# Performance work log

Hardware: AMD Instinct MI355X
Metric: run time of the kernel (lower is better)

Reference implementation:

```python
import jax, jax.numpy as jnp
import numpy as np

B, IN, H0, H1, OUT = 4096, 1024, 4096, 4096, 1024
QMAX = 127.0


def setup_inputs() -> dict:
    key = jax.random.key(0)
    k0, k1, k2, k3 = jax.random.split(key, 4)
    x = jax.random.normal(k0, (B, IN), dtype=jnp.float32)
    # Linear weights hold already-quantized integer values (module casts .int())
    W0 = jax.random.randint(k1, (H0, IN + 1), -127, 128).astype(jnp.int32)
    W1 = jax.random.randint(k2, (H1, H0 + 1), -127, 128).astype(jnp.int32)
    W2 = jax.random.randint(k3, (OUT, H1 + 1), -127, 128).astype(jnp.int32)
    return {
        "x": x,
        "a_in0": jnp.float32(4.0), "a_w0": jnp.float32(0.05),
        "a_in2": jnp.float32(50.0), "a_w2": jnp.float32(0.05),
        "a_in4": jnp.float32(50.0), "a_w4": jnp.float32(0.05),
        "W0": W0, "W1": W1, "W2": W2,
    }


def _quant(x, amax):
    # clamp(round(x * 127/amax), -127, 127) -> int32
    return jnp.clip(jnp.round(x * (QMAX / amax)), -QMAX, QMAX).astype(jnp.int32)


def _qlinear(x, W, a_in, a_w):
    q = _quant(x, a_in)                                   # [B, K] int32
    ones = jnp.ones((q.shape[0], 1), dtype=jnp.int32)     # folded bias column
    q = jnp.concatenate([q, ones], axis=1)                # [B, K+1]
    acc = q @ W.T                                         # int32 GEMM [B, N]
    return acc.astype(jnp.float32) * (a_w * a_in / (QMAX * QMAX))


def reference(x, a_in0, a_w0, a_in2, a_w2, a_in4, a_w4, W0, W1, W2):
    x = x.reshape(x.shape[0], -1)
    x = _qlinear(x, W0, a_in0, a_w0)
    x = jax.nn.relu(x)
    x = _qlinear(x, W1, a_in2, a_w2)
    x = jax.nn.relu(x)
    x = _qlinear(x, W2, a_in4, a_w4)
    return x
```

## Files before the change

kernel.cpp:

```cpp
#include <hip/hip_runtime.h>

#define QMAX 127.0f

typedef int v4i __attribute__((ext_vector_type(4)));

__device__ __forceinline__ void gload_lds16(const void* g, void* l) {
  __builtin_amdgcn_global_load_lds(
      (const __attribute__((address_space(1))) void*)g,
      (__attribute__((address_space(3))) void*)l, 16, 0, 0);
}

__global__ void quant_x_kernel(const float* __restrict__ x,
                               signed char* __restrict__ q,
                               const float* __restrict__ pAin, int n4) {
  int t = blockIdx.x * blockDim.x + threadIdx.x;
  if (t >= n4) return;
  float s = QMAX / pAin[0];
  float4 v = reinterpret_cast<const float4*>(x)[t];
  int q0 = (int)fminf(fmaxf(rintf(v.x * s), -QMAX), QMAX);
  int q1 = (int)fminf(fmaxf(rintf(v.y * s), -QMAX), QMAX);
  int q2 = (int)fminf(fmaxf(rintf(v.z * s), -QMAX), QMAX);
  int q3 = (int)fminf(fmaxf(rintf(v.w * s), -QMAX), QMAX);
  unsigned packed = (unsigned)(q0 & 0xff) | ((unsigned)(q1 & 0xff) << 8) |
                    ((unsigned)(q2 & 0xff) << 16) | ((unsigned)(q3 & 0xff) << 24);
  reinterpret_cast<unsigned*>(q)[t] = packed;
}

__global__ void pack_w_kernel(const int* __restrict__ W,
                              signed char* __restrict__ W8,
                              int* __restrict__ bias,
                              unsigned total, int kshift) {
  unsigned t = blockIdx.x * blockDim.x + threadIdx.x;
  if (t >= total) return;
  unsigned row = t >> kshift;
  unsigned j = t & ((1u << kshift) - 1u);
  unsigned K = 4u << kshift;
  size_t srcBase = (size_t)row * (size_t)(K + 1) + (size_t)j * 4;
  int b0 = W[srcBase + 0], b1 = W[srcBase + 1], b2 = W[srcBase + 2], b3 = W[srcBase + 3];
  unsigned packed = (unsigned)(b0 & 0xff) | ((unsigned)(b1 & 0xff) << 8) |
                    ((unsigned)(b2 & 0xff) << 16) | ((unsigned)(b3 & 0xff) << 24);
  reinterpret_cast<unsigned*>(W8)[t] = packed;
  if (j == 0) bias[row] = W[(size_t)row * (K + 1) + K];
}


#define FENCE() asm volatile("" ::: "memory")
#define BARRIER()                      \
  do {                                 \
    FENCE();                           \
    __builtin_amdgcn_s_barrier();      \
    FENCE();                           \
  } while (0)
#define LGK0() asm volatile("s_waitcnt lgkmcnt(0)" ::: "memory")
#define VMC6() asm volatile("s_waitcnt vmcnt(6)" ::: "memory")
#define VMC0() asm volatile("s_waitcnt vmcnt(0)" ::: "memory")

#define STAGE_A(bf, h, t)                                                     \
  do {                                                                        \
    const signed char* _g = gA + (size_t)((h) * 128) * K + (size_t)(t) * 128; \
    signed char* _l = ldsA + (bf) * 32768 + (h) * 16384 + ldsThr;             \
    gload_lds16(_g, _l);                                                      \
    gload_lds16(_g + (size_t)8 * K, _l + 1024);                               \
  } while (0)

#define STAGE_B(bf, h, t)                                                     \
  do {                                                                        \
    const signed char* _g = gB + (size_t)((h) * 128) * K + (size_t)(t) * 128; \
    signed char* _l = ldsB + (bf) * 32768 + (h) * 16384 + ldsThr;             \
    gload_lds16(_g, _l);                                                      \
    gload_lds16(_g + (size_t)8 * K, _l + 1024);                               \
  } while (0)

#define LDA(bf, qm)                                                           \
  do {                                                                        \
    _Pragma("unroll") for (int m = 0; m < 4; ++m) {                           \
      int row = wm * 128 + (qm) * 64 + m * 16 + l15;                          \
      _Pragma("unroll") for (int kk = 0; kk < 2; ++kk) {                      \
        int off = (kk * 64 + hi * 16) ^ ((row & 7) << 4);                     \
        aR[m][kk] = *(const v4i*)(ldsA + (bf) * 32768 + row * 128 + off);     \
      }                                                                       \
    }                                                                         \
  } while (0)

#define LDB(bf)                                                               \
  do {                                                                        \
    _Pragma("unroll") for (int n = 0; n < 4; ++n) {                           \
      int row = wn * 64 + n * 16 + l15;                                       \
      _Pragma("unroll") for (int kk = 0; kk < 2; ++kk) {                      \
        int off = (kk * 64 + hi * 16) ^ ((row & 7) << 4);                     \
        bR[n][kk] = *(const v4i*)(ldsB + (bf) * 32768 + row * 128 + off);     \
      }                                                                       \
    }                                                                         \
  } while (0)

#define MFMAQ(qm, qn)                                                         \
  do {                                                                        \
    __builtin_amdgcn_s_setprio(1);                                            \
    _Pragma("unroll") for (int m = 0; m < 4; ++m)                             \
    _Pragma("unroll") for (int n = 0; n < 2; ++n)                             \
    _Pragma("unroll") for (int kk = 0; kk < 2; ++kk)                          \
      acc[(qm) * 4 + m][(qn) * 2 + n] = __builtin_amdgcn_mfma_i32_16x16x64_i8(\
          aR[m][kk], bR[(qn) * 2 + n][kk], acc[(qm) * 4 + m][(qn) * 2 + n],   \
          0, 0, 0);                                                           \
    __builtin_amdgcn_s_setprio(0);                                            \
  } while (0)

__global__ __launch_bounds__(512, 2)
void qgemm256_kernel(const signed char* __restrict__ A,
                     const signed char* __restrict__ Bw,
                     const int* __restrict__ bias,
                     signed char* __restrict__ O,
                     int N, int K, int nbn,
                     const float* __restrict__ pAin,
                     const float* __restrict__ pAw,
                     const float* __restrict__ pAnext) {
  extern __shared__ signed char lds[];
  signed char* ldsA = lds;
  signed char* ldsB = lds + 65536;

  const int nwg = gridDim.x, bid = blockIdx.x, per = nwg >> 3;
  const int swz = (bid & 7) * per + (bid >> 3);
  const int brow = swz / nbn, bcol = swz - brow * nbn;
  const int browBase = brow << 8, bcolBase = bcol << 8;

  const int tid = threadIdx.x;
  const int lane = tid & 63, l15 = lane & 15, hi = lane >> 4;
  const int wid = tid >> 6, wm = wid >> 2, wn = wid & 3;

  const int rloc = (wid << 4) + (lane >> 3);
  const int csrc = (lane & 7) ^ ((lane >> 3) & 7);
  const signed char* gA = A + (size_t)(browBase + rloc) * K + csrc * 16;
  const signed char* gB = Bw + (size_t)(bcolBase + rloc) * K + csrc * 16;
  const int ldsThr = (wid << 11) + lane * 16;

  v4i acc[8][4] = {};
  v4i aR[4][2], bR[4][2];

  const int nk = K >> 7, niter = nk >> 1, nkm = nk - 1;

  STAGE_B(0, 0, 0); STAGE_B(0, 1, 0); STAGE_A(0, 0, 0); STAGE_A(0, 1, 0);
  STAGE_B(1, 0, 1); STAGE_B(1, 1, 1); STAGE_A(1, 0, 1);
  VMC6();
  BARRIER();

#pragma unroll 1
  for (int i = 0; i < niter; ++i) {
    const int t1 = 2 * i + 1;
    const int tE = (2 * i + 2) & nkm;
    const int tO = (2 * i + 3) & nkm;
    LDA(0, 0); LDB(0);
    STAGE_A(1, 1, t1);
    BARRIER(); LGK0();
    MFMAQ(0, 0);
    BARRIER();
    STAGE_B(0, 0, tE);
    BARRIER();
    MFMAQ(0, 1);
    BARRIER();
    LDA(0, 1);
    STAGE_B(0, 1, tE);
    BARRIER(); LGK0();
    MFMAQ(1, 0);
    BARRIER();
    STAGE_A(0, 0, tE);
    VMC6();
    BARRIER();
    MFMAQ(1, 1);
    BARRIER();
    LDA(1, 0); LDB(1);
    STAGE_A(0, 1, tE);
    BARRIER(); LGK0();
    MFMAQ(0, 0);
    BARRIER();
    STAGE_B(1, 0, tO);
    BARRIER();
    MFMAQ(0, 1);
    BARRIER();
    LDA(1, 1);
    STAGE_B(1, 1, tO);
    BARRIER(); LGK0();
    MFMAQ(1, 0);
    BARRIER();
    STAGE_A(1, 0, tO);
    VMC6();
    BARRIER();
    MFMAQ(1, 1);
    BARRIER();
  }

  VMC0();

  const float sDeq = (pAw[0] * pAin[0]) / (QMAX * QMAX);
  const float sQ = QMAX / pAnext[0];
#pragma unroll
  for (int nf = 0; nf < 4; ++nf) {
    const int gcol = bcolBase + wn * 64 + nf * 16 + l15;
    const int bv = bias[gcol];
#pragma unroll
    for (int mf = 0; mf < 8; ++mf) {
      const int gr = browBase + wm * 128 + mf * 16 + (hi << 2);
#pragma unroll
      for (int r = 0; r < 4; ++r) {
        float f = (float)(acc[mf][nf][r] + bv) * sDeq;
        f = fmaxf(f, 0.0f);
        float qf = fminf(fmaxf(rintf(f * sQ), -QMAX), QMAX);
        O[(size_t)(gr + r) * N + gcol] = (signed char)(int)qf;
      }
    }
  }
}

template <int MODE>
__global__ __launch_bounds__(256)
void qgemm_kernel(const signed char* __restrict__ A,
                  const signed char* __restrict__ Bw,
                  const int* __restrict__ bias,
                  void* __restrict__ outp,
                  int N, int K, int nbn,
                  const float* __restrict__ pAin,
                  const float* __restrict__ pAw,
                  const float* __restrict__ pAnext) {
  __shared__ signed char slds[32768];
  signed char* ldsA = slds;
  signed char* ldsB = slds + 16384;

  int nwg = gridDim.x;
  int bid = blockIdx.x;
  int per = nwg >> 3;
  int swz = (bid & 7) * per + (bid >> 3);
  int brow = swz / nbn;
  int bcol = swz - brow * nbn;
  int browBase = brow << 7;
  int bcolBase = bcol << 7;

  int tid = threadIdx.x;
  int lane = tid & 63;
  int l15 = lane & 15;
  int hi = lane >> 4;
  int wid = tid >> 6;
  int wr = (wid >> 1) << 6;
  int wc = (wid & 1) << 6;

  v4i acc[4][4] = {};

  int nk = K >> 7;
  for (int kt = 0; kt < nk; ++kt) {
    int k0 = kt << 7;
#pragma unroll
    for (int i = 0; i < 4; ++i) {
      int c = i * 256 + tid;
      int r = c >> 3;
      int osrc = ((c & 7) << 4) ^ ((r & 7) << 4);
      gload_lds16(A + (size_t)(browBase + r) * K + (k0 + osrc), ldsA + c * 16);
      gload_lds16(Bw + (size_t)(bcolBase + r) * K + (k0 + osrc), ldsB + c * 16);
    }
    __syncthreads();
#pragma unroll
    for (int kk = 0; kk < 2; ++kk) {
      v4i a[4], b[4];
#pragma unroll
      for (int m = 0; m < 4; ++m) {
        int row = wr + m * 16 + l15;
        int off = (kk * 64 + hi * 16) ^ ((row & 7) << 4);
        a[m] = *reinterpret_cast<const v4i*>(ldsA + row * 128 + off);
      }
#pragma unroll
      for (int n = 0; n < 4; ++n) {
        int row = wc + n * 16 + l15;
        int off = (kk * 64 + hi * 16) ^ ((row & 7) << 4);
        b[n] = *reinterpret_cast<const v4i*>(ldsB + row * 128 + off);
      }
#pragma unroll
      for (int m = 0; m < 4; ++m)
#pragma unroll
        for (int n = 0; n < 4; ++n)
          acc[m][n] = __builtin_amdgcn_mfma_i32_16x16x64_i8(a[m], b[n], acc[m][n], 0, 0, 0);
    }
    __syncthreads();
  }

  float sDeq = (pAw[0] * pAin[0]) / (QMAX * QMAX);

  if (MODE == 0) {
    float sQ = QMAX / pAnext[0];
    signed char* O = reinterpret_cast<signed char*>(outp);
#pragma unroll
    for (int n = 0; n < 4; ++n) {
      int gcol = bcolBase + wc + n * 16 + l15;
      int bv = bias[gcol];
#pragma unroll
      for (int m = 0; m < 4; ++m) {
        int growb = browBase + wr + m * 16 + (hi << 2);
#pragma unroll
        for (int r = 0; r < 4; ++r) {
          float f = (float)(acc[m][n][r] + bv) * sDeq;
          f = fmaxf(f, 0.0f);
          float qf = fminf(fmaxf(rintf(f * sQ), -QMAX), QMAX);
          O[(size_t)(growb + r) * N + gcol] = (signed char)(int)qf;
        }
      }
    }
  } else {
    float* O = reinterpret_cast<float*>(outp);
#pragma unroll
    for (int n = 0; n < 4; ++n) {
      int gcol = bcolBase + wc + n * 16 + l15;
      int bv = bias[gcol];
#pragma unroll
      for (int m = 0; m < 4; ++m) {
        int growb = browBase + wr + m * 16 + (hi << 2);
#pragma unroll
        for (int r = 0; r < 4; ++r) {
          O[(size_t)(growb + r) * N + gcol] = (float)(acc[m][n][r] + bv) * sDeq;
        }
      }
    }
  }
}

extern "C" void kernel_launch(void* const* d_in, const int* in_sizes, int n_in,
                              void* d_out, int out_size, void* d_ws, size_t ws_size,
                              hipStream_t stream) {
  const float* x     = (const float*)d_in[0];
  const float* a_in0 = (const float*)d_in[1];
  const float* a_w0  = (const float*)d_in[2];
  const float* a_in2 = (const float*)d_in[3];
  const float* a_w2  = (const float*)d_in[4];
  const float* a_in4 = (const float*)d_in[5];
  const float* a_w4  = (const float*)d_in[6];
  const int*   W0    = (const int*)d_in[7];
  const int*   W1    = (const int*)d_in[8];
  const int*   W2    = (const int*)d_in[9];
  float* out = (float*)d_out;

  constexpr int B = 4096, IN = 1024, H0 = 4096, H1 = 4096, OUTN = 1024;

  char* ws = (char*)d_ws;
  size_t off = 0;
  auto alloc = [&](size_t sz) {
    char* p = ws + off;
    off += (sz + 255) & ~(size_t)255;
    return p;
  };
  signed char* qa0 = (signed char*)alloc((size_t)B * IN);
  signed char* qa1 = (signed char*)alloc((size_t)B * H0);
  signed char* qa2 = (signed char*)alloc((size_t)B * H1);
  signed char* W0p = (signed char*)alloc((size_t)H0 * IN);
  signed char* W1p = (signed char*)alloc((size_t)H1 * H0);
  signed char* W2p = (signed char*)alloc((size_t)OUTN * H1);
  int* b0 = (int*)alloc((size_t)H0 * 4);
  int* b1 = (int*)alloc((size_t)H1 * 4);
  int* b2 = (int*)alloc((size_t)OUTN * 4);

  hipFuncSetAttribute((const void*)qgemm256_kernel,
                      hipFuncAttributeMaxDynamicSharedMemorySize, 131072);

  {
    unsigned total0 = (unsigned)H0 * (IN / 4);
    pack_w_kernel<<<(total0 + 255) / 256, 256, 0, stream>>>(W0, W0p, b0, total0, 8);
    unsigned total1 = (unsigned)H1 * (H0 / 4);
    pack_w_kernel<<<(total1 + 255) / 256, 256, 0, stream>>>(W1, W1p, b1, total1, 10);
    unsigned total2 = (unsigned)OUTN * (H1 / 4);
    pack_w_kernel<<<(total2 + 255) / 256, 256, 0, stream>>>(W2, W2p, b2, total2, 10);
  }

  {
    int n4 = B * IN / 4;
    quant_x_kernel<<<(n4 + 255) / 256, 256, 0, stream>>>(x, qa0, a_in0, n4);
  }

  qgemm256_kernel<<<(B / 256) * (H0 / 256), 512, 131072, stream>>>(
      qa0, W0p, b0, qa1, H0, IN, H0 / 256, a_in0, a_w0, a_in2);

  qgemm256_kernel<<<(B / 256) * (H1 / 256), 512, 131072, stream>>>(
      qa1, W1p, b1, qa2, H1, H0, H1 / 256, a_in2, a_w2, a_in4);

  qgemm_kernel<1><<<(B / 128) * (OUTN / 128), 256, 0, stream>>>(
      qa2, W2p, b2, out, OUTN, H1, OUTN / 128, a_in4, a_w4, a_in4);
}
```

Measured before the change: 148.3 us.

## Merge prep kernels into one launch and split GEMM LDS loads by k-half

Folds the three weight-packing kernels and the input quantization kernel into a single prep kernel dispatched by block index, removing three launches and the gaps between them. In the 256-tile GEMM main loop, A fragments are now loaded per k-half into separate register sets, and each MFMA group runs over all four N subtiles for one k-half. LDS reads for the next A quarter are issued before the barrier that precedes the current MFMA group, and the lgkmcnt wait moves after it, so shared-memory loads overlap matrix math. The cost is more live A registers (four sets of four vectors), which may pressure occupancy at two waves per SIMD. The unused MODE template on the small GEMM is also removed.

After: 141.5 us. 1.05x faster.

```diff
diff --git a/kernel.cpp b/kernel.cpp
--- a/kernel.cpp
+++ b/kernel.cpp
@@ -10,37 +10,47 @@
       (__attribute__((address_space(3))) void*)l, 16, 0, 0);
 }
 
-__global__ void quant_x_kernel(const float* __restrict__ x,
-                               signed char* __restrict__ q,
-                               const float* __restrict__ pAin, int n4) {
-  int t = blockIdx.x * blockDim.x + threadIdx.x;
-  if (t >= n4) return;
-  float s = QMAX / pAin[0];
-  float4 v = reinterpret_cast<const float4*>(x)[t];
-  int q0 = (int)fminf(fmaxf(rintf(v.x * s), -QMAX), QMAX);
-  int q1 = (int)fminf(fmaxf(rintf(v.y * s), -QMAX), QMAX);
-  int q2 = (int)fminf(fmaxf(rintf(v.z * s), -QMAX), QMAX);
-  int q3 = (int)fminf(fmaxf(rintf(v.w * s), -QMAX), QMAX);
-  unsigned packed = (unsigned)(q0 & 0xff) | ((unsigned)(q1 & 0xff) << 8) |
-                    ((unsigned)(q2 & 0xff) << 16) | ((unsigned)(q3 & 0xff) << 24);
-  reinterpret_cast<unsigned*>(q)[t] = packed;
-}
-
-__global__ void pack_w_kernel(const int* __restrict__ W,
-                              signed char* __restrict__ W8,
-                              int* __restrict__ bias,
-                              unsigned total, int kshift) {
-  unsigned t = blockIdx.x * blockDim.x + threadIdx.x;
-  if (t >= total) return;
+__device__ __forceinline__ void pack_body(const int* __restrict__ W,
+                                          signed char* __restrict__ W8,
+                                          int* __restrict__ bias,
+                                          unsigned lblk, int kshift) {
+  unsigned t = lblk * 256u + threadIdx.x;
   unsigned row = t >> kshift;
   unsigned j = t & ((1u << kshift) - 1u);
   unsigned K = 4u << kshift;
   size_t srcBase = (size_t)row * (size_t)(K + 1) + (size_t)j * 4;
-  int b0 = W[srcBase + 0], b1 = W[srcBase + 1], b2 = W[srcBase + 2], b3 = W[srcBase + 3];
-  unsigned packed = (unsigned)(b0 & 0xff) | ((unsigned)(b1 & 0xff) << 8) |
-                    ((unsigned)(b2 & 0xff) << 16) | ((unsigned)(b3 & 0xff) << 24);
+  int c0 = W[srcBase + 0], c1 = W[srcBase + 1], c2 = W[srcBase + 2], c3 = W[srcBase + 3];
+  unsigned packed = (unsigned)(c0 & 0xff) | ((unsigned)(c1 & 0xff) << 8) |
+                    ((unsigned)(c2 & 0xff) << 16) | ((unsigned)(c3 & 0xff) << 24);
   reinterpret_cast<unsigned*>(W8)[t] = packed;
   if (j == 0) bias[row] = W[(size_t)row * (K + 1) + K];
+}
+
+__global__ void prep_kernel(const float* __restrict__ x,
+                            signed char* __restrict__ qa0,
+                            const float* __restrict__ pAin,
+                            const int* __restrict__ W0, signed char* __restrict__ W0p, int* __restrict__ b0,
+                            const int* __restrict__ W1, signed char* __restrict__ W1p, int* __restrict__ b1,
+                            const int* __restrict__ W2, signed char* __restrict__ W2p, int* __restrict__ b2) {
+  unsigned blk = blockIdx.x;
+  if (blk < 4096u) {
+    pack_body(W0, W0p, b0, blk, 8);
+  } else if (blk < 20480u) {
+    pack_body(W1, W1p, b1, blk - 4096u, 10);
+  } else if (blk < 24576u) {
+    pack_body(W2, W2p, b2, blk - 20480u, 10);
+  } else {
+    unsigned t = (blk - 24576u) * 256u + threadIdx.x;
+    float s = QMAX / pAin[0];
+    float4 v = reinterpret_cast<const float4*>(x)[t];
+    int q0 = (int)fminf(fmaxf(rintf(v.x * s), -QMAX), QMAX);
+    int q1 = (int)fminf(fmaxf(rintf(v.y * s), -QMAX), QMAX);
+    int q2 = (int)fminf(fmaxf(rintf(v.z * s), -QMAX), QMAX);
+    int q3 = (int)fminf(fmaxf(rintf(v.w * s), -QMAX), QMAX);
+    unsigned packed = (unsigned)(q0 & 0xff) | ((unsigned)(q1 & 0xff) << 8) |
+                      ((unsigned)(q2 & 0xff) << 16) | ((unsigned)(q3 & 0xff) << 24);
+    reinterpret_cast<unsigned*>(qa0)[t] = packed;
+  }
 }
 
 
@@ -71,37 +81,31 @@
     gload_lds16(_g + (size_t)8 * K, _l + 1024);                               \
   } while (0)
 
-#define LDA(bf, qm)                                                           \
+#define LDAQ(bf, qm, kk, dst)                                                 \
   do {                                                                        \
     _Pragma("unroll") for (int m = 0; m < 4; ++m) {                           \
       int row = wm * 128 + (qm) * 64 + m * 16 + l15;                          \
-      _Pragma("unroll") for (int kk = 0; kk < 2; ++kk) {                      \
-        int off = (kk * 64 + hi * 16) ^ ((row & 7) << 4);                     \
-        aR[m][kk] = *(const v4i*)(ldsA + (bf) * 32768 + row * 128 + off);     \
-      }                                                                       \
+      int off = ((kk) * 64 + hi * 16) ^ ((row & 7) << 4);                     \
+      dst[m] = *(const v4i*)(ldsA + (bf) * 32768 + row * 128 + off);          \
     }                                                                         \
   } while (0)
 
-#define LDB(bf)                                                               \
+#define LDBH(bf, kk)                                                          \
   do {                                                                        \
     _Pragma("unroll") for (int n = 0; n < 4; ++n) {                           \
       int row = wn * 64 + n * 16 + l15;                                       \
-      _Pragma("unroll") for (int kk = 0; kk < 2; ++kk) {                      \
-        int off = (kk * 64 + hi * 16) ^ ((row & 7) << 4);                     \
-        bR[n][kk] = *(const v4i*)(ldsB + (bf) * 32768 + row * 128 + off);     \
-      }                                                                       \
+      int off = ((kk) * 64 + hi * 16) ^ ((row & 7) << 4);                     \
+      bR[n][kk] = *(const v4i*)(ldsB + (bf) * 32768 + row * 128 + off);       \
     }                                                                         \
   } while (0)
 
-#define MFMAQ(qm, qn)                                                         \
+#define MFMAQK(qm, kk, asrc)                                                  \
   do {                                                                        \
     __builtin_amdgcn_s_setprio(1);                                            \
     _Pragma("unroll") for (int m = 0; m < 4; ++m)                             \
-    _Pragma("unroll") for (int n = 0; n < 2; ++n)                             \
-    _Pragma("unroll") for (int kk = 0; kk < 2; ++kk)                          \
-      acc[(qm) * 4 + m][(qn) * 2 + n] = __builtin_amdgcn_mfma_i32_16x16x64_i8(\
-          aR[m][kk], bR[(qn) * 2 + n][kk], acc[(qm) * 4 + m][(qn) * 2 + n],   \
-          0, 0, 0);                                                           \
+    _Pragma("unroll") for (int n = 0; n < 4; ++n)                             \
+      acc[(qm) * 4 + m][n] = __builtin_amdgcn_mfma_i32_16x16x64_i8(           \
+          asrc[m], bR[n][kk], acc[(qm) * 4 + m][n], 0, 0, 0);                 \
     __builtin_amdgcn_s_setprio(0);                                            \
   } while (0)
 
@@ -134,7 +138,7 @@
   const int ldsThr = (wid << 11) + lane * 16;
 
   v4i acc[8][4] = {};
-  v4i aR[4][2], bR[4][2];
+  v4i bR[4][2];
 
   const int nk = K >> 7, niter = nk >> 1, nkm = nk - 1;
 
@@ -148,43 +152,50 @@
     const int t1 = 2 * i + 1;
     const int tE = (2 * i + 2) & nkm;
     const int tO = (2 * i + 3) & nkm;
-    LDA(0, 0); LDB(0);
+    v4i a00[4], a01[4], a10[4], a11[4];
+    LDAQ(0, 0, 0, a00); LDBH(0, 0); LDAQ(0, 0, 1, a01); LDBH(0, 1);
     STAGE_A(1, 1, t1);
-    BARRIER(); LGK0();
-    MFMAQ(0, 0);
-    BARRIER();
+    BARRIER();
+    MFMAQK(0, 0, a00);
+    LGK0();
+    BARRIER();
+    LDAQ(0, 1, 0, a10);
     STAGE_B(0, 0, tE);
     BARRIER();
-    MFMAQ(0, 1);
-    BARRIER();
-    LDA(0, 1);
+    MFMAQK(0, 1, a01);
+    BARRIER();
+    LDAQ(0, 1, 1, a11);
     STAGE_B(0, 1, tE);
-    BARRIER(); LGK0();
-    MFMAQ(1, 0);
+    BARRIER();
+    MFMAQK(1, 0, a10);
+    LGK0();
     BARRIER();
     STAGE_A(0, 0, tE);
     VMC6();
     BARRIER();
-    MFMAQ(1, 1);
-    BARRIER();
-    LDA(1, 0); LDB(1);
+    MFMAQK(1, 1, a11);
+    BARRIER();
+    LDAQ(1, 0, 0, a00); LDBH(1, 0); LDAQ(1, 0, 1, a01); LDBH(1, 1);
     STAGE_A(0, 1, tE);
-    BARRIER(); LGK0();
-    MFMAQ(0, 0);
-    BARRIER();
+    BARRIER();
+    MFMAQK(0, 0, a00);
+    LGK0();
+    BARRIER();
+    LDAQ(1, 1, 0, a10);
     STAGE_B(1, 0, tO);
     BARRIER();
-    MFMAQ(0, 1);
-    BARRIER();
-    LDA(1, 1);
+    MFMAQK(0, 1, a01);
+    BARRIER();
+    LDAQ(1, 1, 1, a11);
     STAGE_B(1, 1, tO);
-    BARRIER(); LGK0();
-    MFMAQ(1, 0);
+    BARRIER();
+    MFMAQK(1, 0, a10);
+    LGK0();
     BARRIER();
     STAGE_A(1, 0, tO);
     VMC6();
     BARRIER();
-    MFMAQ(1, 1);
+    MFMAQK(1, 1, a11);
     BARRIER();
   }
 
@@ -210,16 +221,14 @@
   }
 }
 
-template <int MODE>
 __global__ __launch_bounds__(256)
 void qgemm_kernel(const signed char* __restrict__ A,
                   const signed char* __restrict__ Bw,
                   const int* __restrict__ bias,
-                  void* __restrict__ outp,
+                  float* __restrict__ O,
                   int N, int K, int nbn,
                   const float* __restrict__ pAin,
-                  const float* __restrict__ pAw,
-                  const float* __restrict__ pAnext) {
+                  const float* __restrict__ pAw) {
   __shared__ signed char slds[32768];
   signed char* ldsA = slds;
   signed char* ldsB = slds + 16384;
@@ -280,39 +289,16 @@
   }
 
   float sDeq = (pAw[0] * pAin[0]) / (QMAX * QMAX);
-
-  if (MODE == 0) {
-    float sQ = QMAX / pAnext[0];
-    signed char* O = reinterpret_cast<signed char*>(outp);
-#pragma unroll
-    for (int n = 0; n < 4; ++n) {
-      int gcol = bcolBase + wc + n * 16 + l15;
-      int bv = bias[gcol];
-#pragma unroll
-      for (int m = 0; m < 4; ++m) {
-        int growb = browBase + wr + m * 16 + (hi << 2);
-#pragma unroll
-        for (int r = 0; r < 4; ++r) {
-          float f = (float)(acc[m][n][r] + bv) * sDeq;
-          f = fmaxf(f, 0.0f);
-          float qf = fminf(fmaxf(rintf(f * sQ), -QMAX), QMAX);
-          O[(size_t)(growb + r) * N + gcol] = (signed char)(int)qf;
-        }
-      }
-    }
-  } else {
-    float* O = reinterpret_cast<float*>(outp);
-#pragma unroll
-    for (int n = 0; n < 4; ++n) {
-      int gcol = bcolBase + wc + n * 16 + l15;
-      int bv = bias[gcol];
-#pragma unroll
-      for (int m = 0; m < 4; ++m) {
-        int growb = browBase + wr + m * 16 + (hi << 2);
-#pragma unroll
-        for (int r = 0; r < 4; ++r) {
-          O[(size_t)(growb + r) * N + gcol] = (float)(acc[m][n][r] + bv) * sDeq;
-        }
+#pragma unroll
+  for (int n = 0; n < 4; ++n) {
+    int gcol = bcolBase + wc + n * 16 + l15;
+    int bv = bias[gcol];
+#pragma unroll
+    for (int m = 0; m < 4; ++m) {
+      int growb = browBase + wr + m * 16 + (hi << 2);
+#pragma unroll
+      for (int r = 0; r < 4; ++r) {
+        O[(size_t)(growb + r) * N + gcol] = (float)(acc[m][n][r] + bv) * sDeq;
       }
     }
   }
@@ -355,19 +341,10 @@
   hipFuncSetAttribute((const void*)qgemm256_kernel,
                       hipFuncAttributeMaxDynamicSharedMemorySize, 131072);
 
-  {
-    unsigned total0 = (unsigned)H0 * (IN / 4);
-    pack_w_kernel<<<(total0 + 255) / 256, 256, 0, stream>>>(W0, W0p, b0, total0, 8);
-    unsigned total1 = (unsigned)H1 * (H0 / 4);
-    pack_w_kernel<<<(total1 + 255) / 256, 256, 0, stream>>>(W1, W1p, b1, total1, 10);
-    unsigned total2 = (unsigned)OUTN * (H1 / 4);
-    pack_w_kernel<<<(total2 + 255) / 256, 256, 0, stream>>>(W2, W2p, b2, total2, 10);
-  }
-
-  {
-    int n4 = B * IN / 4;
-    quant_x_kernel<<<(n4 + 255) / 256, 256, 0, stream>>>(x, qa0, a_in0, n4);
-  }
+  prep_kernel<<<28672, 256, 0, stream>>>(x, qa0, a_in0,
+                                         W0, W0p, b0,
+                                         W1, W1p, b1,
+                                         W2, W2p, b2);
 
   qgemm256_kernel<<<(B / 256) * (H0 / 256), 512, 131072, stream>>>(
       qa0, W0p, b0, qa1, H0, IN, H0 / 256, a_in0, a_w0, a_in2);
@@ -375,6 +352,6 @@
   qgemm256_kernel<<<(B / 256) * (H1 / 256), 512, 131072, stream>>>(
       qa1, W1p, b1, qa2, H1, H0, H1 / 256, a_in2, a_w2, a_in4);
 
-  qgemm_kernel<1><<<(B / 128) * (OUTN / 128), 256, 0, stream>>>(
-      qa2, W2p, b2, out, OUTN, H1, OUTN / 128, a_in4, a_w4, a_in4);
-}
+  qgemm_kernel<<<(B / 128) * (OUTN / 128), 256, 0, stream>>>(
+      qa2, W2p, b2, out, OUTN, H1, OUTN / 128, a_in4, a_w4);
+}
```
